# Performance work log

Hardware: AMD Instinct MI355X
Metric: run time of the kernel (lower is better)

The kernel has to match this reference:

```python
import jax, jax.numpy as jnp
import numpy as np

B, S, E, H = 2, 2048, 1024, 8
DH = E // H


def setup_inputs() -> dict:
    key = jax.random.key(0)
    ks = jax.random.split(key, 8)
    sc = 1.0 / np.sqrt(E)
    return {
        "q": jax.random.normal(ks[0], (B, S, E), jnp.float32),
        "k": jax.random.normal(ks[1], (B, S, E), jnp.float32),
        "v": jax.random.normal(ks[2], (B, S, E), jnp.float32),
        "Wq": jax.random.normal(ks[3], (E, E), jnp.float32) * sc,
        "bq": jnp.zeros((E,), jnp.float32),
        "Wk": jax.random.normal(ks[4], (E, E), jnp.float32) * sc,
        "bk": jnp.zeros((E,), jnp.float32),
        "Wv": jax.random.normal(ks[5], (E, E), jnp.float32) * sc,
        "bv": jnp.zeros((E,), jnp.float32),
        "Wo": jax.random.normal(ks[6], (E, E), jnp.float32) * sc,
        "bo": jnp.zeros((E,), jnp.float32),
        "is_causal": 1,
    }


def reference(q, k, v, Wq, bq, Wk, bk, Wv, bv, Wo, bo, is_causal):
    # q,k,v: [B,S,E]. Dense projections, split into H heads of dim DH.
    def heads(x, W, b):
        y = x @ W + b                       # [B,S,E]
        return y.reshape(B, S, H, DH).transpose(0, 2, 1, 3)  # [B,H,S,DH]

    qh = heads(q, Wq, bq)
    kh = heads(k, Wk, bk)
    vh = heads(v, Wv, bv)

    scale = 1.0 / jnp.sqrt(jnp.asarray(DH, q.dtype))
    scores = jnp.einsum("bhsd,bhtd->bhst", qh, kh) * scale  # [B,H,S,S]

    if is_causal:
        # tril mask (BigBird layout is all-ones here; causality comes from attn_mask)
        causal = jnp.tril(jnp.ones((S, S), bool))
        neg = jnp.asarray(jnp.finfo(scores.dtype).min, scores.dtype)
        scores = jnp.where(causal[None, None], scores, neg)

    attn = jax.nn.softmax(scores, axis=-1)                  # [B,H,S,S]
    ctx = jnp.einsum("bhst,bhtd->bhsd", attn, vh)           # [B,H,S,DH]
    ctx = ctx.transpose(0, 2, 1, 3).reshape(B, S, E)        # merge heads
    return ctx @ Wo + bo
```

## Files before the change

kernel.cpp:

```cpp
#include <hip/hip_runtime.h>
#include <math.h>


typedef __bf16 bf16_t;
typedef __bf16 bf16x8 __attribute__((ext_vector_type(8)));
typedef float f32x4 __attribute__((ext_vector_type(4)));

#define MFMA16(a, b, c) __builtin_amdgcn_mfma_f32_16x16x32_bf16(a, b, c, 0, 0, 0)

__device__ __forceinline__ void gld16(const bf16_t* g, bf16_t* l) {
  __builtin_amdgcn_global_load_lds(
      (const __attribute__((address_space(1))) void*)g,
      (__attribute__((address_space(3))) void*)l, 16, 0, 0);
}

__global__ __launch_bounds__(256) void wtrans(const float* W0, const float* W1,
                                              const float* W2, const float* W3,
                                              bf16_t* out) {
  const float* W = (blockIdx.z == 0) ? W0 : (blockIdx.z == 1) ? W1
                                          : (blockIdx.z == 2) ? W2 : W3;
  bf16_t* o = out + (size_t)blockIdx.z * 1024 * 1024;
  __shared__ float t[32][33];
  int n0 = blockIdx.x * 32, k0 = blockIdx.y * 32;
  int tx = threadIdx.x, ty = threadIdx.y;
#pragma unroll
  for (int i = 0; i < 4; i++)
    t[ty + 8 * i][tx] = W[(size_t)(k0 + ty + 8 * i) * 1024 + n0 + tx];
  __syncthreads();
#pragma unroll
  for (int i = 0; i < 4; i++)
    o[(size_t)(n0 + ty + 8 * i) * 1024 + k0 + tx] = (bf16_t)t[tx][ty + 8 * i];
}

__global__ __launch_bounds__(256) void conv_k(const float* q, const float* k,
                                              const float* v, bf16_t* qb,
                                              bf16_t* kb, bf16_t* vb) {
  const float* x = (blockIdx.y == 0) ? q : (blockIdx.y == 1) ? k : v;
  bf16_t* y = (blockIdx.y == 0) ? qb : (blockIdx.y == 1) ? kb : vb;
  size_t i = ((size_t)blockIdx.x * 256 + threadIdx.x) * 8;
  float4 a = *(const float4*)(x + i);
  float4 b = *(const float4*)(x + i + 4);
  bf16x8 o = {(bf16_t)a.x, (bf16_t)a.y, (bf16_t)a.z, (bf16_t)a.w,
              (bf16_t)b.x, (bf16_t)b.y, (bf16_t)b.z, (bf16_t)b.w};
  *(bf16x8*)(y + i) = o;
}

template <int MODE>
__global__ __launch_bounds__(256) void gemm_k(
    const bf16_t* qb, const bf16_t* kb, const bf16_t* vb, const bf16_t* Wt,
    const float* b0, const float* b1, const float* b2, bf16_t* Qh, bf16_t* Kh,
    bf16_t* Vt, float* Of32) {
  __shared__ bf16_t As[128 * 64];
  __shared__ bf16_t Bs[128 * 64];
  const int tid = threadIdx.x, w = tid >> 6, lane = tid & 63;
  const int bm = blockIdx.y, bn = blockIdx.x;
  const int wr = w >> 1, wc = w & 1, q4 = lane >> 4, lo = lane & 15;
  const int z = (MODE == 0) ? blockIdx.z : 3;
  const bf16_t* A = (MODE == 1) ? qb : (z == 0) ? qb : (z == 1) ? kb : vb;
  const bf16_t* Bt = Wt + (size_t)z * 1024 * 1024;
  const float* bias = (MODE == 1) ? b0 : (z == 0) ? b0 : (z == 1) ? b1 : b2;

  f32x4 acc[4][4];
#pragma unroll
  for (int m = 0; m < 4; m++)
#pragma unroll
    for (int n = 0; n < 4; n++) acc[m][n] = (f32x4){0.f, 0.f, 0.f, 0.f};

  const int lr = lane >> 3, lc = lane & 7;
  const int scol = (lc ^ lr) * 8;

  for (int k0 = 0; k0 < 1024; k0 += 64) {
#pragma unroll
    for (int c = 0; c < 4; c++) {
      int row = w * 32 + c * 8;
      gld16(A + (size_t)(bm * 128 + row + lr) * 1024 + k0 + scol, &As[row * 64]);
      gld16(Bt + (size_t)(bn * 128 + row + lr) * 1024 + k0 + scol, &Bs[row * 64]);
    }
    __syncthreads();
#pragma unroll
    for (int kc = 0; kc < 2; kc++) {
      bf16x8 af[4], bfr[4];
#pragma unroll
      for (int m = 0; m < 4; m++) {
        int rr = wr * 64 + m * 16 + lo;
        af[m] = *(const bf16x8*)&As[rr * 64 + ((kc * 4 + q4) ^ (rr & 7)) * 8];
      }
#pragma unroll
      for (int n = 0; n < 4; n++) {
        int rr = wc * 64 + n * 16 + lo;
        bfr[n] = *(const bf16x8*)&Bs[rr * 64 + ((kc * 4 + q4) ^ (rr & 7)) * 8];
      }
#pragma unroll
      for (int m = 0; m < 4; m++)
#pragma unroll
        for (int n = 0; n < 4; n++)
          acc[m][n] = MFMA16(af[m], bfr[n], acc[m][n]);
    }
    __syncthreads();
  }

#pragma unroll
  for (int m = 0; m < 4; m++) {
#pragma unroll
    for (int n = 0; n < 4; n++) {
      int rowg0 = bm * 128 + wr * 64 + m * 16 + q4 * 4;
      int colg = bn * 128 + wc * 64 + n * 16 + lo;
      float bv = bias[colg];
#pragma unroll
      for (int rg = 0; rg < 4; rg++) {
        float val = acc[m][n][rg] + bv;
        int row = rowg0 + rg;
        if (MODE == 1) {
          Of32[(size_t)row * 1024 + colg] = val;
        } else {
          int b = row >> 11, s = row & 2047;
          int h = colg >> 7, d = colg & 127;
          if (z == 0)
            Qh[(((size_t)(b * 8 + h)) * 2048 + s) * 128 + d] = (bf16_t)val;
          else if (z == 1)
            Kh[(((size_t)(b * 8 + h)) * 2048 + s) * 128 + d] = (bf16_t)val;
          else
            Vt[(((size_t)(b * 8 + h)) * 128 + d) * 2048 + s] = (bf16_t)val;
        }
      }
    }
  }
}

__global__ __launch_bounds__(256) void flash_k(const bf16_t* Qh,
                                               const bf16_t* Kh,
                                               const bf16_t* Vt, bf16_t* ctx,
                                               const int* causal_p) {
  __shared__ bf16_t sm[32768 + 4 * 1280];
  const int tid = threadIdx.x, w = tid >> 6, lane = tid & 63;
  const int q4 = lane >> 4, lo = lane & 15;
  const int n0 = blockIdx.x;
  const int u = n0 & 255, hi = n0 >> 8;
  const int bh = u & 15, p0 = u >> 4;
  const int t = hi ? (31 - p0) : p0;
  const int causal = *causal_p;
  const int kmax = causal ? t : 31;

  bf16_t* Ps = sm + 32768 + w * 1280;

  bf16x8 aq[4];
  {
    const bf16_t* qa = Qh + ((size_t)bh * 2048 + t * 64 + w * 16 + lo) * 128;
#pragma unroll
    for (int ks = 0; ks < 4; ks++) aq[ks] = *(const bf16x8*)(qa + ks * 32 + q4 * 8);
  }

  const bf16_t* Kbase = Kh + (size_t)bh * 2048 * 128;
  const bf16_t* Vbase = Vt + (size_t)bh * 128 * 2048;
  const int kr = tid >> 2, kc = (tid & 3) * 4;
  const int vd = tid >> 1, vc = (tid & 1) * 4;

  bf16x8 kreg[4], vreg[4];
  auto loadKV = [&](int kt) {
    const bf16_t* kp = Kbase + (size_t)(kt * 64 + kr) * 128;
    const bf16_t* vp = Vbase + (size_t)vd * 2048 + kt * 64;
#pragma unroll
    for (int i = 0; i < 4; i++) {
      kreg[i] = *(const bf16x8*)(kp + (kc + i) * 8);
      vreg[i] = *(const bf16x8*)(vp + (vc + i) * 8);
    }
  };

  f32x4 acc[8], lacc;
#pragma unroll
  for (int i = 0; i < 8; i++) acc[i] = (f32x4){0.f, 0.f, 0.f, 0.f};
  lacc = (f32x4){0.f, 0.f, 0.f, 0.f};

  const bf16_t one = (bf16_t)1.0f;
  const bf16x8 vone = {one, one, one, one, one, one, one, one};
  const float sc2 = 0.08838834764831845f * 1.44269504088896f;

  loadKV(0);
  for (int kt = 0; kt <= kmax; ++kt) {
    bf16_t* Kd = sm + (kt & 1) * 8192;
    bf16_t* Vd = sm + 16384 + (kt & 1) * 8192;
#pragma unroll
    for (int i = 0; i < 4; i++)
      *(bf16x8*)&Kd[kr * 128 + (((kc + i) ^ (kr & 7)) * 8)] = kreg[i];
#pragma unroll
    for (int i = 0; i < 4; i++)
      *(bf16x8*)&Vd[vd * 64 + (((vc + i) ^ ((vd >> 1) & 7)) * 8)] = vreg[i];
    if (kt < kmax) loadKV(kt + 1);
    __syncthreads();

    f32x4 sa[4];
#pragma unroll
    for (int nt = 0; nt < 4; nt++) sa[nt] = (f32x4){0.f, 0.f, 0.f, 0.f};
#pragma unroll
    for (int ks = 0; ks < 4; ks++) {
#pragma unroll
      for (int nt = 0; nt < 4; nt++) {
        int key = nt * 16 + lo;
        bf16x8 bk =
            *(const bf16x8*)&Kd[key * 128 + (((ks * 4 + q4) ^ (key & 7)) * 8)];
        sa[nt] = MFMA16(aq[ks], bk, sa[nt]);
      }
    }

    const bool diag = causal && (kt == t);
    const int rloc = w * 16 + q4 * 4;
#pragma unroll
    for (int nt = 0; nt < 4; nt++) {
      int key = nt * 16 + lo;
#pragma unroll
      for (int rg = 0; rg < 4; rg++) {
        float pv = exp2f(sa[nt][rg] * sc2);
        if (diag && key > rloc + rg) pv = 0.f;
        Ps[(q4 * 4 + rg) * 80 + key] = (bf16_t)pv;
      }
    }

    bf16x8 ap0 = *(const bf16x8*)&Ps[lo * 80 + q4 * 8];
    bf16x8 ap1 = *(const bf16x8*)&Ps[lo * 80 + 32 + q4 * 8];
    lacc = MFMA16(ap0, vone, lacc);
    lacc = MFMA16(ap1, vone, lacc);
#pragma unroll
    for (int n = 0; n < 8; n++) {
      int d = n * 16 + lo;
      int sw = (d >> 1) & 7;
      bf16x8 bv0 = *(const bf16x8*)&Vd[d * 64 + ((q4 ^ sw) * 8)];
      bf16x8 bv1 = *(const bf16x8*)&Vd[d * 64 + (((4 + q4) ^ sw) * 8)];
      acc[n] = MFMA16(ap0, bv0, acc[n]);
      acc[n] = MFMA16(ap1, bv1, acc[n]);
    }
  }

  int b = bh >> 3, h = bh & 7;
#pragma unroll
  for (int rg = 0; rg < 4; rg++) {
    float inv = 1.f / lacc[rg];
    int r = b * 2048 + t * 64 + w * 16 + q4 * 4 + rg;
#pragma unroll
    for (int n = 0; n < 8; n++)
      ctx[(size_t)r * 1024 + h * 128 + n * 16 + lo] = (bf16_t)(acc[n][rg] * inv);
  }
}

extern "C" void kernel_launch(void* const* d_in, const int* in_sizes, int n_in,
                              void* d_out, int out_size, void* d_ws,
                              size_t ws_size, hipStream_t stream) {
  const float* q = (const float*)d_in[0];
  const float* k = (const float*)d_in[1];
  const float* v = (const float*)d_in[2];
  const float* Wq = (const float*)d_in[3];
  const float* bq = (const float*)d_in[4];
  const float* Wk = (const float*)d_in[5];
  const float* bk = (const float*)d_in[6];
  const float* Wv = (const float*)d_in[7];
  const float* bv = (const float*)d_in[8];
  const float* Wo = (const float*)d_in[9];
  const float* bo = (const float*)d_in[10];
  const int* isc = (const int*)d_in[11];

  char* ws = (char*)d_ws;
  bf16_t* Wt = (bf16_t*)ws;
  bf16_t* qb = (bf16_t*)(ws + (8ull << 20));
  bf16_t* kb = (bf16_t*)(ws + (16ull << 20));
  bf16_t* vb = (bf16_t*)(ws + (24ull << 20));
  bf16_t* Qh = (bf16_t*)(ws + (32ull << 20));
  bf16_t* Kh = (bf16_t*)(ws + (40ull << 20));
  bf16_t* Vt = (bf16_t*)(ws + (48ull << 20));
  bf16_t* ctx = (bf16_t*)(ws + (8ull << 20));

  wtrans<<<dim3(32, 32, 4), dim3(32, 8), 0, stream>>>(Wq, Wk, Wv, Wo, Wt);
  conv_k<<<dim3(2048, 3), 256, 0, stream>>>(q, k, v, qb, kb, vb);

  gemm_k<0><<<dim3(8, 32, 3), 256, 0, stream>>>(qb, kb, vb, Wt, bq, bk, bv, Qh,
                                                Kh, Vt, nullptr);

  flash_k<<<dim3(512), 256, 0, stream>>>(Qh, Kh, Vt, ctx, isc);

  gemm_k<1><<<dim3(8, 32), 256, 0, stream>>>(ctx, nullptr, nullptr, Wt, bo,
                                             nullptr, nullptr, nullptr, nullptr,
                                             nullptr, (float*)d_out);
}
```

Measured before the change: 249.9 us.

## Double-buffer GEMM LDS tiles with BK=32 to overlap loads and MFMA

New measurement: 245.6 us. No clear change (-1.7%).

```diff
diff --git a/kernel.cpp b/kernel.cpp
--- a/kernel.cpp
+++ b/kernel.cpp
@@ -50,8 +50,8 @@
     const bf16_t* qb, const bf16_t* kb, const bf16_t* vb, const bf16_t* Wt,
     const float* b0, const float* b1, const float* b2, bf16_t* Qh, bf16_t* Kh,
     bf16_t* Vt, float* Of32) {
-  __shared__ bf16_t As[128 * 64];
-  __shared__ bf16_t Bs[128 * 64];
+  __shared__ bf16_t As[2][128 * 32];
+  __shared__ bf16_t Bs[2][128 * 32];
   const int tid = threadIdx.x, w = tid >> 6, lane = tid & 63;
   const int bm = blockIdx.y, bn = blockIdx.x;
   const int wr = w >> 1, wc = w & 1, q4 = lane >> 4, lo = lane & 15;
@@ -66,36 +66,41 @@
 #pragma unroll
     for (int n = 0; n < 4; n++) acc[m][n] = (f32x4){0.f, 0.f, 0.f, 0.f};
 
-  const int lr = lane >> 3, lc = lane & 7;
-  const int scol = (lc ^ lr) * 8;
-
-  for (int k0 = 0; k0 < 1024; k0 += 64) {
-#pragma unroll
-    for (int c = 0; c < 4; c++) {
-      int row = w * 32 + c * 8;
-      gld16(A + (size_t)(bm * 128 + row + lr) * 1024 + k0 + scol, &As[row * 64]);
-      gld16(Bt + (size_t)(bn * 128 + row + lr) * 1024 + k0 + scol, &Bs[row * 64]);
-    }
-    __syncthreads();
-#pragma unroll
-    for (int kc = 0; kc < 2; kc++) {
-      bf16x8 af[4], bfr[4];
-#pragma unroll
-      for (int m = 0; m < 4; m++) {
-        int rr = wr * 64 + m * 16 + lo;
-        af[m] = *(const bf16x8*)&As[rr * 64 + ((kc * 4 + q4) ^ (rr & 7)) * 8];
-      }
-#pragma unroll
-      for (int n = 0; n < 4; n++) {
-        int rr = wc * 64 + n * 16 + lo;
-        bfr[n] = *(const bf16x8*)&Bs[rr * 64 + ((kc * 4 + q4) ^ (rr & 7)) * 8];
-      }
-#pragma unroll
-      for (int m = 0; m < 4; m++)
-#pragma unroll
-        for (int n = 0; n < 4; n++)
-          acc[m][n] = MFMA16(af[m], bfr[n], acc[m][n]);
-    }
+  const int sr = lane >> 2, sc = lane & 3;
+
+  auto stage = [&](int k0, int b) {
+#pragma unroll
+    for (int g = 0; g < 2; g++) {
+      int rbase = w * 32 + g * 16;
+      int r = rbase + sr;
+      int cg = (sc ^ (r & 3)) * 8;
+      gld16(A + (size_t)(bm * 128 + r) * 1024 + k0 + cg, &As[b][rbase * 32]);
+      gld16(Bt + (size_t)(bn * 128 + r) * 1024 + k0 + cg, &Bs[b][rbase * 32]);
+    }
+  };
+
+  stage(0, 0);
+  __syncthreads();
+
+  for (int k = 0; k < 32; k++) {
+    int cur = k & 1;
+    if (k < 31) stage((k + 1) * 32, 1 - cur);
+
+    bf16x8 af[4], bfr[4];
+#pragma unroll
+    for (int m = 0; m < 4; m++) {
+      int rr = wr * 64 + m * 16 + lo;
+      af[m] = *(const bf16x8*)&As[cur][rr * 32 + ((q4 ^ (rr & 3)) * 8)];
+    }
+#pragma unroll
+    for (int n = 0; n < 4; n++) {
+      int rr = wc * 64 + n * 16 + lo;
+      bfr[n] = *(const bf16x8*)&Bs[cur][rr * 32 + ((q4 ^ (rr & 3)) * 8)];
+    }
+#pragma unroll
+    for (int m = 0; m < 4; m++)
+#pragma unroll
+      for (int n = 0; n < 4; n++) acc[m][n] = MFMA16(af[m], bfr[n], acc[m][n]);
     __syncthreads();
   }
 
```

## Double-buffer GEMM tiles via register prefetch and merge prep kernels

Applied to the files above, without the earlier changes.

New measurement: 236.2 us. -5.5%, faster.

```diff
diff --git a/kernel.cpp b/kernel.cpp
--- a/kernel.cpp
+++ b/kernel.cpp
@@ -8,41 +8,39 @@
 
 #define MFMA16(a, b, c) __builtin_amdgcn_mfma_f32_16x16x32_bf16(a, b, c, 0, 0, 0)
 
-__device__ __forceinline__ void gld16(const bf16_t* g, bf16_t* l) {
-  __builtin_amdgcn_global_load_lds(
-      (const __attribute__((address_space(1))) void*)g,
-      (__attribute__((address_space(3))) void*)l, 16, 0, 0);
-}
-
-__global__ __launch_bounds__(256) void wtrans(const float* W0, const float* W1,
-                                              const float* W2, const float* W3,
-                                              bf16_t* out) {
-  const float* W = (blockIdx.z == 0) ? W0 : (blockIdx.z == 1) ? W1
-                                          : (blockIdx.z == 2) ? W2 : W3;
-  bf16_t* o = out + (size_t)blockIdx.z * 1024 * 1024;
-  __shared__ float t[32][33];
-  int n0 = blockIdx.x * 32, k0 = blockIdx.y * 32;
-  int tx = threadIdx.x, ty = threadIdx.y;
-#pragma unroll
-  for (int i = 0; i < 4; i++)
-    t[ty + 8 * i][tx] = W[(size_t)(k0 + ty + 8 * i) * 1024 + n0 + tx];
-  __syncthreads();
-#pragma unroll
-  for (int i = 0; i < 4; i++)
-    o[(size_t)(n0 + ty + 8 * i) * 1024 + k0 + tx] = (bf16_t)t[tx][ty + 8 * i];
-}
-
-__global__ __launch_bounds__(256) void conv_k(const float* q, const float* k,
-                                              const float* v, bf16_t* qb,
-                                              bf16_t* kb, bf16_t* vb) {
-  const float* x = (blockIdx.y == 0) ? q : (blockIdx.y == 1) ? k : v;
-  bf16_t* y = (blockIdx.y == 0) ? qb : (blockIdx.y == 1) ? kb : vb;
-  size_t i = ((size_t)blockIdx.x * 256 + threadIdx.x) * 8;
-  float4 a = *(const float4*)(x + i);
-  float4 b = *(const float4*)(x + i + 4);
-  bf16x8 o = {(bf16_t)a.x, (bf16_t)a.y, (bf16_t)a.z, (bf16_t)a.w,
-              (bf16_t)b.x, (bf16_t)b.y, (bf16_t)b.z, (bf16_t)b.w};
-  *(bf16x8*)(y + i) = o;
+__global__ __launch_bounds__(256) void prep(const float* q, const float* k,
+                                            const float* v, bf16_t* qb,
+                                            bf16_t* kb, bf16_t* vb,
+                                            const float* W0, const float* W1,
+                                            const float* W2, const float* W3,
+                                            bf16_t* Wt) {
+  const int bid = blockIdx.x, tid = threadIdx.x;
+  if (bid < 6144) {
+    const int z = bid >> 11, chunk = bid & 2047;
+    const float* x = (z == 0) ? q : (z == 1) ? k : v;
+    bf16_t* y = (z == 0) ? qb : (z == 1) ? kb : vb;
+    size_t i = ((size_t)chunk * 256 + tid) * 8;
+    float4 a = *(const float4*)(x + i);
+    float4 b = *(const float4*)(x + i + 4);
+    bf16x8 o = {(bf16_t)a.x, (bf16_t)a.y, (bf16_t)a.z, (bf16_t)a.w,
+                (bf16_t)b.x, (bf16_t)b.y, (bf16_t)b.z, (bf16_t)b.w};
+    *(bf16x8*)(y + i) = o;
+  } else {
+    __shared__ float t[32][33];
+    const int b2 = bid - 6144;
+    const int wz = b2 >> 10, t2 = b2 & 1023;
+    const float* W = (wz == 0) ? W0 : (wz == 1) ? W1 : (wz == 2) ? W2 : W3;
+    bf16_t* o = Wt + (size_t)wz * 1024 * 1024;
+    const int n0 = (t2 & 31) * 32, k0 = (t2 >> 5) * 32;
+    const int tx = tid & 31, ty = tid >> 5;
+#pragma unroll
+    for (int i = 0; i < 4; i++)
+      t[ty + 8 * i][tx] = W[(size_t)(k0 + ty + 8 * i) * 1024 + n0 + tx];
+    __syncthreads();
+#pragma unroll
+    for (int i = 0; i < 4; i++)
+      o[(size_t)(n0 + ty + 8 * i) * 1024 + k0 + tx] = (bf16_t)t[tx][ty + 8 * i];
+  }
 }
 
 template <int MODE>
@@ -50,8 +48,8 @@
     const bf16_t* qb, const bf16_t* kb, const bf16_t* vb, const bf16_t* Wt,
     const float* b0, const float* b1, const float* b2, bf16_t* Qh, bf16_t* Kh,
     bf16_t* Vt, float* Of32) {
-  __shared__ bf16_t As[128 * 64];
-  __shared__ bf16_t Bs[128 * 64];
+  __shared__ bf16_t As[2][128 * 64];
+  __shared__ bf16_t Bs[2][128 * 64];
   const int tid = threadIdx.x, w = tid >> 6, lane = tid & 63;
   const int bm = blockIdx.y, bn = blockIdx.x;
   const int wr = w >> 1, wc = w & 1, q4 = lane >> 4, lo = lane & 15;
@@ -66,29 +64,43 @@
 #pragma unroll
     for (int n = 0; n < 4; n++) acc[m][n] = (f32x4){0.f, 0.f, 0.f, 0.f};
 
-  const int lr = lane >> 3, lc = lane & 7;
-  const int scol = (lc ^ lr) * 8;
-
-  for (int k0 = 0; k0 < 1024; k0 += 64) {
-#pragma unroll
-    for (int c = 0; c < 4; c++) {
-      int row = w * 32 + c * 8;
-      gld16(A + (size_t)(bm * 128 + row + lr) * 1024 + k0 + scol, &As[row * 64]);
-      gld16(Bt + (size_t)(bn * 128 + row + lr) * 1024 + k0 + scol, &Bs[row * 64]);
-    }
+  const int r2 = tid >> 1;
+  const int cb = (tid & 1) * 4;
+  const bf16_t* Arow = A + (size_t)(bm * 128 + r2) * 1024;
+  const bf16_t* Brow = Bt + (size_t)(bn * 128 + r2) * 1024;
+
+  bf16x8 ar[4], br[4];
+  auto loadAB = [&](int k0) {
+#pragma unroll
+    for (int i = 0; i < 4; i++) {
+      ar[i] = *(const bf16x8*)(Arow + k0 + (cb + i) * 8);
+      br[i] = *(const bf16x8*)(Brow + k0 + (cb + i) * 8);
+    }
+  };
+
+  loadAB(0);
+  for (int k = 0; k < 16; k++) {
+    const int cur = k & 1;
+#pragma unroll
+    for (int i = 0; i < 4; i++) {
+      *(bf16x8*)&As[cur][r2 * 64 + (((cb + i) ^ (r2 & 7)) * 8)] = ar[i];
+      *(bf16x8*)&Bs[cur][r2 * 64 + (((cb + i) ^ (r2 & 7)) * 8)] = br[i];
+    }
+    if (k < 15) loadAB((k + 1) * 64);
     __syncthreads();
+
 #pragma unroll
     for (int kc = 0; kc < 2; kc++) {
       bf16x8 af[4], bfr[4];
 #pragma unroll
       for (int m = 0; m < 4; m++) {
         int rr = wr * 64 + m * 16 + lo;
-        af[m] = *(const bf16x8*)&As[rr * 64 + ((kc * 4 + q4) ^ (rr & 7)) * 8];
+        af[m] = *(const bf16x8*)&As[cur][rr * 64 + (((kc * 4 + q4) ^ (rr & 7)) * 8)];
       }
 #pragma unroll
       for (int n = 0; n < 4; n++) {
         int rr = wc * 64 + n * 16 + lo;
-        bfr[n] = *(const bf16x8*)&Bs[rr * 64 + ((kc * 4 + q4) ^ (rr & 7)) * 8];
+        bfr[n] = *(const bf16x8*)&Bs[cur][rr * 64 + (((kc * 4 + q4) ^ (rr & 7)) * 8)];
       }
 #pragma unroll
       for (int m = 0; m < 4; m++)
@@ -96,7 +108,6 @@
         for (int n = 0; n < 4; n++)
           acc[m][n] = MFMA16(af[m], bfr[n], acc[m][n]);
     }
-    __syncthreads();
   }
 
 #pragma unroll
@@ -267,8 +278,7 @@
   bf16_t* Vt = (bf16_t*)(ws + (48ull << 20));
   bf16_t* ctx = (bf16_t*)(ws + (8ull << 20));
 
-  wtrans<<<dim3(32, 32, 4), dim3(32, 8), 0, stream>>>(Wq, Wk, Wv, Wo, Wt);
-  conv_k<<<dim3(2048, 3), 256, 0, stream>>>(q, k, v, qb, kb, vb);
+  prep<<<dim3(10240), 256, 0, stream>>>(q, k, v, qb, kb, vb, Wq, Wk, Wv, Wo, Wt);
 
   gemm_k<0><<<dim3(8, 32, 3), 256, 0, stream>>>(qb, kb, vb, Wt, bq, bk, bv, Qh,
                                                 Kh, Vt, nullptr);
```
